# Performance work log

Measured on AMD Instinct MI355X. Metric: run time of the kernel, lower is better.

Reference implementation:

```python
import jax, jax.numpy as jnp
import numpy as np
import math

B, H, N, D = 2, 16, 2048, 128
SM_SCALE = 1.0 / math.sqrt(D)


def setup_inputs() -> dict:
    key = jax.random.key(0)
    kq, kk, kv = jax.random.split(key, 3)
    q = jax.random.normal(kq, (B, H, N, D), dtype=jnp.float32)
    k = jax.random.normal(kk, (B, H, N, D), dtype=jnp.float32)
    v = jax.random.normal(kv, (B, H, N, D), dtype=jnp.float32)
    return {"q": q, "k": k, "v": v}


def reference(q, k, v):
    # RBF-kernel causal attention (non-softmax):
    #   logits_ij = -sm_scale * ||q_i - k_j||^2
    #            = 2*sm_scale*q_i.k_j - sm_scale*||q_i||^2 - sm_scale*||k_j||^2
    #   p = exp(logits) with causal mask (p_ij = 0 for j > i); out = p @ v
    sm_scale = jnp.float32(SM_SCALE)
    q_sq = sm_scale * jnp.sum(q * q, axis=-1)  # [B,H,N]
    k_sq = sm_scale * jnp.sum(k * k, axis=-1)  # [B,H,N]
    qk = jnp.einsum("bhmd,bhnd->bhmn", q, k)
    logits = (2.0 * sm_scale) * qk - q_sq[..., :, None] - k_sq[..., None, :]
    n = q.shape[2]
    causal = jnp.tril(jnp.ones((n, n), dtype=bool))
    logits = jnp.where(causal, logits, -jnp.inf)
    p = jnp.exp(logits)  # NOT normalized (non-softmax attention)
    out = jnp.einsum("bhmn,bhnd->bhmd", p, v)
    return out
```

## Files before the change

### kernel.cpp

```cpp
#include <hip/hip_runtime.h>
#include <math.h>


#define NSEQ 2048
#define DH   128
#define BHC  32
#define SM_SCALE 0.08838834764831845f

typedef __attribute__((ext_vector_type(8))) short    short8;
typedef __attribute__((ext_vector_type(8))) _Float16 half8;
typedef __attribute__((ext_vector_type(4))) short    short4_;
typedef __attribute__((ext_vector_type(4))) float    float4_;
typedef __attribute__((ext_vector_type(4))) unsigned uint4_;
typedef __attribute__((ext_vector_type(2))) unsigned uint2_;

#define KST 136
#define VST 72
#define PST 72

__device__ __forceinline__ short f2bf(float x){
  union{float f; unsigned u;} a; a.f=x;
  unsigned r = a.u + 0x7fffu + ((a.u>>16)&1u);
  return (short)(r>>16);
}
__device__ __forceinline__ float bf2f(short h){
  union{float f; unsigned u;} a; a.u=((unsigned)(unsigned short)h)<<16; return a.f;
}
__device__ __forceinline__ unsigned packbf(float a, float b){
  return (unsigned)(unsigned short)f2bf(a) | ((unsigned)(unsigned short)f2bf(b)<<16);
}
__device__ __forceinline__ unsigned cvtpk_bf16(float a, float b){
  unsigned r;
  asm("v_cvt_pk_bf16_f32 %0, %1, %2" : "=v"(r) : "v"(a), "v"(b));
  return r;
}

__global__ __launch_bounds__(256)
void prep_kv5(const float* __restrict__ kg, const float* __restrict__ vg,
              _Float16* __restrict__ khg, short* __restrict__ vtg,
              float* __restrict__ ksqg){
  __shared__ unsigned Vls[128*33];
  const int b = blockIdx.x, t = threadIdx.x;
  const int l = t & 63, wv = t >> 6;
  if(b < 1024){
    const int bh = b>>5, jt = b&31;
    const float4_* vb4 = (const float4_*)(vg + ((size_t)bh*NSEQ + (size_t)jt*64)*DH);
    #pragma unroll
    for(int i=0;i<8;++i){
      float4_ own = vb4[i*256 + t];
      float4_ par;
      par.x = __shfl_xor(own.x, 32); par.y = __shfl_xor(own.y, 32);
      par.z = __shfl_xor(own.z, 32); par.w = __shfl_xor(own.w, 32);
      const int hi = (l>>5)&1;
      unsigned w0 = hi ? packbf(par.z, own.z) : packbf(own.x, par.x);
      unsigned w1 = hi ? packbf(par.w, own.w) : packbf(own.y, par.y);
      const int dd = 4*(t&31) + 2*hi;
      const int j2 = 4*i + wv;
      Vls[dd*33 + j2]     = w0;
      Vls[(dd+1)*33 + j2] = w1;
    }
    __syncthreads();
    short* outp = vtg + ((size_t)(bh*32 + jt)*DH)*64;
    #pragma unroll
    for(int it=0; it<4; ++it){
      int idx = t + 256*it;
      int d = idx>>3, slot = idx&7;
      uint4_ o;
      o.x = Vls[d*33 + 4*slot];   o.y = Vls[d*33 + 4*slot+1];
      o.z = Vls[d*33 + 4*slot+2]; o.w = Vls[d*33 + 4*slot+3];
      *(uint4_*)(outp + d*64 + 8*slot) = o;
    }
  } else {
    const int kb = b - 1024;
    const float4_* kb4 = (const float4_*)(kg + (size_t)kb*64*DH);
    #pragma unroll
    for(int i=0;i<8;++i){
      float4_ x = kb4[i*256 + t];
      const int row = 64*kb + 8*i + (t>>5);
      const int d   = 4*(t&31);
      union{ _Float16 h[4]; uint2_ u; } pk;
      pk.h[0]=(_Float16)x.x; pk.h[1]=(_Float16)x.y;
      pk.h[2]=(_Float16)x.z; pk.h[3]=(_Float16)x.w;
      *(uint2_*)(khg + (size_t)row*DH + d) = pk.u;
      float ss = x.x*x.x + x.y*x.y + x.z*x.z + x.w*x.w;
      ss += __shfl_xor(ss,1);  ss += __shfl_xor(ss,2);
      ss += __shfl_xor(ss,4);  ss += __shfl_xor(ss,8);
      ss += __shfl_xor(ss,16);
      if((l&31)==0) ksqg[row] = SM_SCALE*ss;
    }
  }
}

__global__ __launch_bounds__(256,3)
void rbf_attn6(const float* __restrict__ qg,
               const _Float16* __restrict__ khg,
               const short* __restrict__ vtg,
               const float* __restrict__ ksqg,
               float* __restrict__ og){
  __shared__ short Kst[64*KST];
  __shared__ short Vst[128*VST];
  __shared__ short Pls[4*16*PST];
  __shared__ float ksLs[64];

  const int tid=threadIdx.x;
  const int w=tid>>6, l=tid&63;
  const int quad=l>>4, lr=l&15;
  const int bh=blockIdx.x;
  const int mq = 31 - blockIdx.y;
  const int qbase = 64*mq + 16*w;

  const float*    Qg = qg   + (size_t)bh*NSEQ*DH;
  const _Float16* Kh = khg  + (size_t)bh*NSEQ*DH;
  const short*    Vt = vtg  + (size_t)bh*32*DH*64;
  const float*    Ks = ksqg + (size_t)bh*NSEQ;
  float*          Og = og   + (size_t)bh*NSEQ*DH;
  short* Pw = Pls + w*16*PST;

  half8 qf[4];
  float qsq;
  {
    const int qrow = qbase + lr;
    const float* qp = Qg + (size_t)qrow*DH + 8*quad;
    float ss=0.f;
    #pragma unroll
    for(int ks=0;ks<4;++ks){
      float4_ a = *(const float4_*)(qp + 32*ks);
      float4_ b = *(const float4_*)(qp + 32*ks + 4);
      half8 h;
      #pragma unroll
      for(int j=0;j<4;++j){
        h[j]   = (_Float16)a[j];
        h[j+4] = (_Float16)b[j];
        ss += a[j]*a[j] + b[j]*b[j];
      }
      qf[ks]=h;
    }
    ss += __shfl_xor(ss,16);
    ss += __shfl_xor(ss,32);
    qsq = SM_SCALE*ss;
  }

  float4_ oacc[8];
  #pragma unroll
  for(int b2=0;b2<8;++b2) oacc[b2] = (float4_)0.f;

  uint4_ kreg[4], vreg[4];
  float  kqreg = 0.f;
  {
    #pragma unroll
    for(int it=0;it<4;++it){
      int idx = tid + 256*it;
      int row = idx>>4, c = idx&15;
      kreg[it] = *(const uint4_*)(Kh + (size_t)row*DH + 8*c);
      int d = idx>>3, slot = idx&7;
      vreg[it] = *(const uint4_*)(Vt + (size_t)d*64 + 8*slot);
    }
    if(tid<64) kqreg = Ks[tid];
  }

  for(int jt=0; jt<=mq; ++jt){
    #pragma unroll
    for(int it=0;it<4;++it){
      int idx = tid + 256*it;
      int row = idx>>4, c = idx&15;
      *(uint4_*)&Kst[row*KST + 8*c] = kreg[it];
      int d = idx>>3, slot = idx&7;
      *(uint4_*)&Vst[d*VST + 8*slot] = vreg[it];
    }
    if(tid<64) ksLs[tid] = kqreg;
    __syncthreads();

    if(jt < mq){
      const int jc2 = (jt+1)*64;
      #pragma unroll
      for(int it=0;it<4;++it){
        int idx = tid + 256*it;
        int row = idx>>4, c = idx&15;
        kreg[it] = *(const uint4_*)(Kh + (size_t)(jc2+row)*DH + 8*c);
        int d = idx>>3, slot = idx&7;
        vreg[it] = *(const uint4_*)(Vt + ((size_t)(jt+1)*DH + d)*64 + 8*slot);
      }
      if(tid<64) kqreg = Ks[jc2 + tid];
    }

    float4_ sacc[4];
    #pragma unroll
    for(int ct=0;ct<4;++ct) sacc[ct] = (float4_)0.f;

    __builtin_amdgcn_s_setprio(1);
    #pragma unroll
    for(int ks=0;ks<4;++ks){
      half8 kf[4];
      #pragma unroll
      for(int ct=0;ct<4;++ct)
        kf[ct] = *(const half8*)&Kst[(16*ct+lr)*KST + 32*ks + 8*quad];
      #pragma unroll
      for(int ct=0;ct<4;++ct)
        sacc[ct]=__builtin_amdgcn_mfma_f32_16x16x32_f16(kf[ct],qf[ks],sacc[ct],0,0,0);
    }
    __builtin_amdgcn_s_setprio(0);

    {
      const int jg0 = 64*jt;
      const int qrow = qbase + lr;
      #pragma unroll
      for(int ct=0;ct<4;++ct){
        float4_ kq = *(const float4_*)&ksLs[16*ct + 4*quad];
        const int j0 = jg0 + 16*ct + 4*quad;
        float p[4];
        #pragma unroll
        for(int r=0;r<4;++r){
          float logit = (2.f*SM_SCALE)*sacc[ct][r] - qsq - kq[r];
          p[r] = (j0 + r <= qrow) ? __expf(logit) : 0.f;
        }
        uint2_ pw;
        pw.x = cvtpk_bf16(p[0], p[1]);
        pw.y = cvtpk_bf16(p[2], p[3]);
        *(uint2_*)&Pw[lr*PST + 16*ct + 4*quad] = pw;
      }
    }

    __builtin_amdgcn_s_setprio(1);
    #pragma unroll
    for(int ks2=0;ks2<2;++ks2){
      const short8 pf = *(const short8*)&Pw[lr*PST + 32*ks2 + 8*quad];
      #pragma unroll
      for(int ctv=0;ctv<8;++ctv){
        const short8 vf = *(const short8*)&Vst[(16*ctv+lr)*VST + 32*ks2 + 8*quad];
        oacc[ctv]=__builtin_amdgcn_mfma_f32_16x16x32_bf16(pf,vf,oacc[ctv],0,0,0);
      }
    }
    __builtin_amdgcn_s_setprio(0);

    __syncthreads();
  }

  #pragma unroll
  for(int ctv=0;ctv<8;++ctv)
    #pragma unroll
    for(int r=0;r<4;++r){
      const int qrow = qbase + 4*quad + r;
      Og[(size_t)qrow*DH + 16*ctv + lr] = oacc[ctv][r];
    }
}

#define KSTf 136
#define VSTf 36
#define PSTf 72

__global__ __launch_bounds__(256,2)
void rbf_attn_mfma(const float* __restrict__ qg, const float* __restrict__ kg,
                   const float* __restrict__ vg, float* __restrict__ og){
  __shared__ short    Khi[64*KSTf];
  __shared__ short    Klo[64*KSTf];
  __shared__ unsigned VP [128*VSTf];
  __shared__ short    Pfb[64*PSTf];
  __shared__ float    qsq_s[64];
  __shared__ float    ksq_s[64];

  const int tid=threadIdx.x;
  const int w=tid>>6, l=tid&63;
  const int wr=w>>1, wc=w&1;
  const int quad=l>>4, lr=l&15;
  const int bh=blockIdx.x, yp=blockIdx.y;

  const float* Qg = qg + (size_t)bh*NSEQ*DH;
  const float* Kg = kg + (size_t)bh*NSEQ*DH;
  const float* Vg = vg + (size_t)bh*NSEQ*DH;
  float*       Og = og + (size_t)bh*NSEQ*DH;

  for(int pass=0;pass<2;++pass){
    const int m = pass ? (31-yp) : yp;
    __syncthreads();
    short8 qhf[2][4], qlf[2][4];
    #pragma unroll
    for(int rt=0;rt<2;++rt){
      const int grow = m*64 + 32*wr + 16*rt + lr;
      const float* qp = Qg + (size_t)grow*DH + 8*quad;
      float ss=0.f;
      #pragma unroll
      for(int ks=0;ks<4;++ks){
        float4_ a = *(const float4_*)(qp + 32*ks);
        float4_ b = *(const float4_*)(qp + 32*ks + 4);
        short8 hi, lo;
        #pragma unroll
        for(int j=0;j<4;++j){
          float fa=a[j], fb=b[j];
          short ha=f2bf(fa); hi[j]=ha;   lo[j]=f2bf(fa-bf2f(ha));
          short hb=f2bf(fb); hi[j+4]=hb; lo[j+4]=f2bf(fb-bf2f(hb));
          ss += fa*fa + fb*fb;
        }
        qhf[rt][ks]=hi; qlf[rt][ks]=lo;
      }
      ss += __shfl_xor(ss,16);
      ss += __shfl_xor(ss,32);
      if(wc==0 && quad==0) qsq_s[32*wr+16*rt+lr] = SM_SCALE*ss;
    }
    float4_ oacc[2][4];
    #pragma unroll
    for(int a=0;a<2;++a)
      #pragma unroll
      for(int b=0;b<4;++b) oacc[a][b] = (float4_)0.f;

    const int ntiles = m+1;
    for(int jt=0;jt<ntiles;++jt){
      const int jc = jt*64;
      __syncthreads();
      #pragma unroll
      for(int it=0;it<4;++it){
        const int i = tid + 256*it;
        const int row = i>>4, c0 = 8*(i&15);
        const float* kp = Kg + (size_t)(jc+row)*DH + c0;
        float4_ a = *(const float4_*)kp;
        float4_ b = *(const float4_*)(kp+4);
        short8 hi, lo;
        float ss=0.f;
        #pragma unroll
        for(int j=0;j<4;++j){
          float fa=a[j], fb=b[j];
          short ha=f2bf(fa); hi[j]=ha;   lo[j]=f2bf(fa-bf2f(ha));
          short hb=f2bf(fb); hi[j+4]=hb; lo[j+4]=f2bf(fb-bf2f(hb));
          ss += fa*fa + fb*fb;
        }
        ss += __shfl_xor(ss,1); ss += __shfl_xor(ss,2);
        ss += __shfl_xor(ss,4); ss += __shfl_xor(ss,8);
        if(lr==0) ksq_s[row] = SM_SCALE*ss;
        *(short8*)&Khi[row*KSTf + c0] = hi;
        *(short8*)&Klo[row*KSTf + c0] = lo;
      }
      #pragma unroll
      for(int it=0;it<4;++it){
        const int u = tid + 256*it;
        const int d = u & 127, jg = u >> 7;
        const float* vp = Vg + (size_t)(jc + 8*jg)*DH + d;
        float vv[8];
        #pragma unroll
        for(int jj=0;jj<8;++jj) vv[jj] = vp[(size_t)jj*DH];
        uint4_ pk;
        #pragma unroll
        for(int p2=0;p2<4;++p2)
          pk[p2] = (unsigned)(unsigned short)f2bf(vv[2*p2]) |
                   ((unsigned)(unsigned short)f2bf(vv[2*p2+1])<<16);
        *(uint4_*)&VP[d*VSTf + 4*jg] = pk;
      }
      __syncthreads();
      float4_ sacc[2][2];
      #pragma unroll
      for(int a=0;a<2;++a)
        #pragma unroll
        for(int b=0;b<2;++b) sacc[a][b] = (float4_)0.f;
      #pragma unroll
      for(int ks=0;ks<4;++ks){
        short8 khf[2], klf[2];
        #pragma unroll
        for(int ct=0;ct<2;++ct){
          const int off = (32*wc + 16*ct + lr)*KSTf + 32*ks + 8*quad;
          khf[ct] = *(const short8*)&Khi[off];
          klf[ct] = *(const short8*)&Klo[off];
        }
        #pragma unroll
        for(int rt=0;rt<2;++rt)
          #pragma unroll
          for(int ct=0;ct<2;++ct){
            sacc[rt][ct]=__builtin_amdgcn_mfma_f32_16x16x32_bf16(qhf[rt][ks],khf[ct],sacc[rt][ct],0,0,0);
            sacc[rt][ct]=__builtin_amdgcn_mfma_f32_16x16x32_bf16(qhf[rt][ks],klf[ct],sacc[rt][ct],0,0,0);
            sacc[rt][ct]=__builtin_amdgcn_mfma_f32_16x16x32_bf16(qlf[rt][ks],khf[ct],sacc[rt][ct],0,0,0);
          }
      }
      #pragma unroll
      for(int rt=0;rt<2;++rt){
        float qs[4];
        #pragma unroll
        for(int r=0;r<4;++r) qs[r]=qsq_s[32*wr+16*rt+4*quad+r];
        #pragma unroll
        for(int ct=0;ct<2;++ct){
          const float ksq = ksq_s[32*wc+16*ct+lr];
          const int colg = jc + 32*wc+16*ct+lr;
          #pragma unroll
          for(int r=0;r<4;++r){
            const int rowg = m*64 + 32*wr+16*rt+4*quad+r;
            float logit = (2.f*SM_SCALE)*sacc[rt][ct][r] - qs[r] - ksq;
            float p = (colg<=rowg)? __expf(logit) : 0.f;
            Pfb[(32*wr+16*rt+4*quad+r)*PSTf + 32*wc+16*ct+lr] = f2bf(p);
          }
        }
      }
      __syncthreads();
      #pragma unroll
      for(int ks2=0;ks2<2;++ks2){
        short8 pf[2];
        #pragma unroll
        for(int rt=0;rt<2;++rt)
          pf[rt] = *(const short8*)&Pfb[(32*wr+16*rt+lr)*PSTf + 32*ks2 + 8*quad];
        #pragma unroll
        for(int ctv=0;ctv<4;++ctv){
          const int d = 64*wc + 16*ctv + lr;
          const short8 vfb = *(const short8*)((const short*)VP + d*(2*VSTf) + 32*ks2 + 8*quad);
          #pragma unroll
          for(int rt=0;rt<2;++rt)
            oacc[rt][ctv]=__builtin_amdgcn_mfma_f32_16x16x32_bf16(pf[rt],vfb,oacc[rt][ctv],0,0,0);
        }
      }
    }
    #pragma unroll
    for(int rt=0;rt<2;++rt)
      #pragma unroll
      for(int ctv=0;ctv<4;++ctv)
        #pragma unroll
        for(int r=0;r<4;++r){
          const int rowg = m*64 + 32*wr + 16*rt + 4*quad + r;
          Og[(size_t)rowg*DH + 64*wc + 16*ctv + lr] = oacc[rt][ctv][r];
        }
  }
}

extern "C" void kernel_launch(void* const* d_in, const int* in_sizes, int n_in,
                              void* d_out, int out_size, void* d_ws, size_t ws_size,
                              hipStream_t stream) {
  const float* q = (const float*)d_in[0];
  const float* k = (const float*)d_in[1];
  const float* v = (const float*)d_in[2];
  float* out = (float*)d_out;

  const size_t nElem = (size_t)BHC*NSEQ*DH;
  const size_t need  = nElem*2*sizeof(short) + (size_t)BHC*NSEQ*sizeof(float);

  if(ws_size >= need){
    _Float16* khg = (_Float16*)d_ws;
    short*    vtg = (short*)(khg + nElem);
    float*    ksqg = (float*)(vtg + nElem);
    prep_kv5<<<2048, 256, 0, stream>>>(k, v, khg, vtg, ksqg);
    rbf_attn6<<<dim3(BHC,32), 256, 0, stream>>>(q, khg, vtg, ksqg, out);
  } else {
    rbf_attn_mfma<<<dim3(BHC,16), 256, 0, stream>>>(q, k, v, out);
  }
}
```

Measured before the change: 196.8 us.

## Keep P in registers via permlane swaps, skip masked diagonal tiles, reorder blocks

Drops the shared-memory staging of the probability tile. The S accumulator layout is now rearranged into the MFMA A-operand layout in registers, using permlane32/permlane16 swaps (with a ds_swizzle fallback). On the diagonal tile, each wave skips QK MFMAs and PV steps whose columns are fully masked. Launch bounds go from 3 to 4 blocks per CU, using the freed LDS, and the query-tile order becomes a serpentine grouping instead of longest-first. This removes LDS write/read traffic and wasted diagonal work, at the cost of more register pressure and a less clean longest-first balance.

```diff
diff --git a/kernel.cpp b/kernel.cpp
--- a/kernel.cpp
+++ b/kernel.cpp
@@ -16,7 +16,6 @@
 
 #define KST 136
 #define VST 72
-#define PST 72
 
 __device__ __forceinline__ short f2bf(float x){
   union{float f; unsigned u;} a; a.f=x;
@@ -33,6 +32,22 @@
   unsigned r;
   asm("v_cvt_pk_bf16_f32 %0, %1, %2" : "=v"(r) : "v"(a), "v"(b));
   return r;
+}
+
+__device__ __forceinline__ void qswap32(unsigned A, unsigned B, unsigned &X, unsigned &Y){
+  uint2_ r = __builtin_amdgcn_permlane32_swap(A, B, false, false);
+  X = r[0]; Y = r[1];
+}
+__device__ __forceinline__ void qswap16(unsigned A, unsigned B, unsigned &X, unsigned &Y, int oddq){
+#if __has_builtin(__builtin_amdgcn_permlane16_swap)
+  uint2_ r = __builtin_amdgcn_permlane16_swap(A, B, false, false);
+  X = r[0]; Y = r[1];
+#else
+  unsigned As = (unsigned)__builtin_amdgcn_ds_swizzle((int)A, 0x401F);
+  unsigned Bs = (unsigned)__builtin_amdgcn_ds_swizzle((int)B, 0x401F);
+  X = oddq ? Bs : A;
+  Y = oddq ? B  : As;
+#endif
 }
 
 __global__ __launch_bounds__(256)
@@ -91,22 +106,23 @@
   }
 }
 
-__global__ __launch_bounds__(256,3)
-void rbf_attn6(const float* __restrict__ qg,
+__global__ __launch_bounds__(256,4)
+void rbf_attn7(const float* __restrict__ qg,
                const _Float16* __restrict__ khg,
                const short* __restrict__ vtg,
                const float* __restrict__ ksqg,
                float* __restrict__ og){
   __shared__ short Kst[64*KST];
   __shared__ short Vst[128*VST];
-  __shared__ short Pls[4*16*PST];
   __shared__ float ksLs[64];
 
   const int tid=threadIdx.x;
   const int w=tid>>6, l=tid&63;
   const int quad=l>>4, lr=l&15;
   const int bh=blockIdx.x;
-  const int mq = 31 - blockIdx.y;
+  const int y = blockIdx.y;
+  const int g = y>>3, z = y&7;
+  const int mq = g*8 + ((g&1) ? (7-z) : z);
   const int qbase = 64*mq + 16*w;
 
   const float*    Qg = qg   + (size_t)bh*NSEQ*DH;
@@ -114,7 +130,6 @@
   const short*    Vt = vtg  + (size_t)bh*32*DH*64;
   const float*    Ks = ksqg + (size_t)bh*NSEQ;
   float*          Og = og   + (size_t)bh*NSEQ*DH;
-  short* Pw = Pls + w*16*PST;
 
   half8 qf[4];
   float qsq;
@@ -183,6 +198,10 @@
       if(tid<64) kqreg = Ks[jc2 + tid];
     }
 
+    const bool diag = (jt == mq);
+    const int ctmax = diag ? w : 3;
+    const int nks2  = (diag && w < 2) ? 1 : 2;
+
     float4_ sacc[4];
     #pragma unroll
     for(int ct=0;ct<4;++ct) sacc[ct] = (float4_)0.f;
@@ -193,41 +212,52 @@
       half8 kf[4];
       #pragma unroll
       for(int ct=0;ct<4;++ct)
-        kf[ct] = *(const half8*)&Kst[(16*ct+lr)*KST + 32*ks + 8*quad];
+        if(ct<=ctmax) kf[ct] = *(const half8*)&Kst[(16*ct+lr)*KST + 32*ks + 8*quad];
       #pragma unroll
       for(int ct=0;ct<4;++ct)
-        sacc[ct]=__builtin_amdgcn_mfma_f32_16x16x32_f16(kf[ct],qf[ks],sacc[ct],0,0,0);
+        if(ct<=ctmax) sacc[ct]=__builtin_amdgcn_mfma_f32_16x16x32_f16(kf[ct],qf[ks],sacc[ct],0,0,0);
     }
     __builtin_amdgcn_s_setprio(0);
 
+    unsigned pk[4][2];
     {
       const int jg0 = 64*jt;
       const int qrow = qbase + lr;
       #pragma unroll
       for(int ct=0;ct<4;++ct){
-        float4_ kq = *(const float4_*)&ksLs[16*ct + 4*quad];
-        const int j0 = jg0 + 16*ct + 4*quad;
-        float p[4];
-        #pragma unroll
-        for(int r=0;r<4;++r){
-          float logit = (2.f*SM_SCALE)*sacc[ct][r] - qsq - kq[r];
-          p[r] = (j0 + r <= qrow) ? __expf(logit) : 0.f;
-        }
-        uint2_ pw;
-        pw.x = cvtpk_bf16(p[0], p[1]);
-        pw.y = cvtpk_bf16(p[2], p[3]);
-        *(uint2_*)&Pw[lr*PST + 16*ct + 4*quad] = pw;
+        if(ct < 2*nks2){
+          float4_ kq = *(const float4_*)&ksLs[16*ct + 4*quad];
+          const int j0 = jg0 + 16*ct + 4*quad;
+          float p[4];
+          #pragma unroll
+          for(int r=0;r<4;++r){
+            float logit = (2.f*SM_SCALE)*sacc[ct][r] - qsq - kq[r];
+            p[r] = (j0 + r <= qrow) ? __expf(logit) : 0.f;
+          }
+          pk[ct][0] = cvtpk_bf16(p[0], p[1]);
+          pk[ct][1] = cvtpk_bf16(p[2], p[3]);
+        }
       }
     }
 
     __builtin_amdgcn_s_setprio(1);
     #pragma unroll
     for(int ks2=0;ks2<2;++ks2){
-      const short8 pf = *(const short8*)&Pw[lr*PST + 32*ks2 + 8*quad];
-      #pragma unroll
-      for(int ctv=0;ctv<8;++ctv){
-        const short8 vf = *(const short8*)&Vst[(16*ctv+lr)*VST + 32*ks2 + 8*quad];
-        oacc[ctv]=__builtin_amdgcn_mfma_f32_16x16x32_bf16(pf,vf,oacc[ctv],0,0,0);
+      if(ks2 < nks2){
+        unsigned A0,B0,A1,B1;
+        qswap32(pk[2*ks2][0], pk[2*ks2+1][0], A0, B0);
+        qswap32(pk[2*ks2][1], pk[2*ks2+1][1], A1, B1);
+        unsigned w0,w1,w2,w3;
+        qswap16(A0, B0, w0, w2, quad&1);
+        qswap16(A1, B1, w1, w3, quad&1);
+        union{ uint4_ u; short8 s; } pfu;
+        pfu.u.x=w0; pfu.u.y=w1; pfu.u.z=w2; pfu.u.w=w3;
+        const short8 pf = pfu.s;
+        #pragma unroll
+        for(int ctv=0;ctv<8;++ctv){
+          const short8 vf = *(const short8*)&Vst[(16*ctv+lr)*VST + 32*ks2 + 8*quad];
+          oacc[ctv]=__builtin_amdgcn_mfma_f32_16x16x32_bf16(pf,vf,oacc[ctv],0,0,0);
+        }
       }
     }
     __builtin_amdgcn_s_setprio(0);
@@ -430,7 +460,7 @@
     short*    vtg = (short*)(khg + nElem);
     float*    ksqg = (float*)(vtg + nElem);
     prep_kv5<<<2048, 256, 0, stream>>>(k, v, khg, vtg, ksqg);
-    rbf_attn6<<<dim3(BHC,32), 256, 0, stream>>>(q, khg, vtg, ksqg, out);
+    rbf_attn7<<<dim3(BHC,32), 256, 0, stream>>>(q, khg, vtg, ksqg, out);
   } else {
     rbf_attn_mfma<<<dim3(BHC,16), 256, 0, stream>>>(q, k, v, out);
   }
```

After: 299.9 us. 1.52x slower.
